# Kernel tuning notes

Hardware: AMD Instinct MI355X
Metric: run time of the kernel (lower is better)

## Reference

```python
import jax, jax.numpy as jnp
import numpy as np

N_EMBD = 512
Q_N_EMBD = 512
N_HEAD = 8
EPS = 1e-5


def _layernorm(x, w, b):
    mu = jnp.mean(x, axis=-1, keepdims=True)
    var = jnp.mean(jnp.square(x - mu), axis=-1, keepdims=True)
    return (x - mu) * jax.lax.rsqrt(var + EPS) * w + b


def setup_inputs() -> dict:
    key = jax.random.key(0)
    ks = jax.random.split(key, 16)
    B, C, H, W = 8, N_EMBD, 32, 32
    s = 1.0 / np.sqrt(N_EMBD)
    inp = {
        "q": jax.random.normal(ks[0], (B, Q_N_EMBD, H, W), jnp.float32),
        "kv": jax.random.normal(ks[1], (B, C, H, W), jnp.float32),
        "ln_kv_w": jnp.ones((N_EMBD,), jnp.float32),
        "ln_kv_b": jnp.zeros((N_EMBD,), jnp.float32),
        "ln_q_w": jnp.ones((Q_N_EMBD,), jnp.float32),
        "ln_q_b": jnp.zeros((Q_N_EMBD,), jnp.float32),
        "Wk": jax.random.normal(ks[2], (N_EMBD, N_EMBD), jnp.float32) * s,
        "bk": jnp.zeros((N_EMBD,), jnp.float32),
        "Wq": jax.random.normal(ks[3], (Q_N_EMBD, N_EMBD), jnp.float32) * s,
        "bq": jnp.zeros((N_EMBD,), jnp.float32),
        "Wv": jax.random.normal(ks[4], (N_EMBD, N_EMBD), jnp.float32) * s,
        "bv": jnp.zeros((N_EMBD,), jnp.float32),
        "Wp": jax.random.normal(ks[5], (N_EMBD, N_EMBD), jnp.float32) * s,
        "bp": jnp.zeros((N_EMBD,), jnp.float32),
    }
    return inp


def reference(q, kv, ln_kv_w, ln_kv_b, ln_q_w, ln_q_b,
              Wk, bk, Wq, bq, Wv, bv, Wp, bp):
    B, C, H, W = kv.shape
    c_q = q.shape[1]
    T = H * W
    hd = C // N_HEAD  # head dim

    # [B, C, H, W] -> [B, T, C] tokens
    kv_t = kv.reshape(B, C, T).transpose(0, 2, 1)
    q_t = q.reshape(B, c_q, T).transpose(0, 2, 1)

    kv_n = _layernorm(kv_t, ln_kv_w, ln_kv_b)
    q_n = _layernorm(q_t, ln_q_w, ln_q_b)

    # projections, split heads: [B, T, C] -> [B, H, T, hd]
    def heads(x):
        return x.reshape(B, T, N_HEAD, hd).transpose(0, 2, 1, 3)

    k = heads(kv_n @ Wk + bk)
    qh = heads(q_n @ Wq + bq)
    v = heads(kv_n @ Wv + bv)

    att = jnp.einsum('bhqd,bhkd->bhqk', qh, k) * (1.0 / np.sqrt(hd))
    att = jax.nn.softmax(att, axis=-1)
    y = jnp.einsum('bhqk,bhkd->bhqd', att, v)
    y = y.transpose(0, 2, 1, 3).reshape(B, T, C)
    y = y @ Wp + bp

    x = kv_t + y  # residual on (pre-LN) kv tokens
    return x.transpose(0, 2, 1).reshape(B, C, H, W)
```

## Files before the change

kernel.cpp:

```cpp
#include <hip/hip_runtime.h>
#include <stdint.h>

#define DI static __device__ __forceinline__

typedef __attribute__((ext_vector_type(8))) short bh8;
typedef __attribute__((ext_vector_type(4))) float f4;

DI short f2bf(float f) {
  unsigned u = __float_as_uint(f);
  u += 0x7fffu + ((u >> 16) & 1u);
  return (short)(u >> 16);
}

DI unsigned pkbf(float a, float b) {
  unsigned ua = __float_as_uint(a) + 0x8000u;
  unsigned ub = __float_as_uint(b) + 0x8000u;
  return __builtin_amdgcn_perm(ub, ua, 0x07060302u);
}

DI unsigned pk4fp8(float a, float b, float c, float d) {
  unsigned w = 0;
  w = __builtin_amdgcn_cvt_pk_fp8_f32(a, b, w, false);
  w = __builtin_amdgcn_cvt_pk_fp8_f32(c, d, w, true);
  return w;
}

DI void gll16(const void* g, void* l) {
  __builtin_amdgcn_global_load_lds(
      (const __attribute__((address_space(1))) unsigned int*)g,
      (__attribute__((address_space(3))) unsigned int*)l, 16, 0, 0);
}

DI f4 mfma16(bh8 a, bh8 b, f4 c) {
  return __builtin_amdgcn_mfma_f32_16x16x32_bf16(a, b, c, 0, 0, 0);
}

DI f4 mfma8(long a, long b, f4 c) {
  return __builtin_amdgcn_mfma_f32_16x16x32_fp8_fp8(a, b, c, 0, 0, 0);
}

DI bh8 ld8(const short* p) { return *(const bh8*)p; }

__global__ __launch_bounds__(256) void prep_k(
    const float* __restrict__ kv, const float* __restrict__ qi,
    const float* __restrict__ kw, const float* __restrict__ kbv,
    const float* __restrict__ qw, const float* __restrict__ qbv,
    const float* __restrict__ Wk, const float* __restrict__ Wq,
    const float* __restrict__ Wv, const float* __restrict__ Wp,
    short* __restrict__ kvn, short* __restrict__ qn,
    short* __restrict__ Wt)
{
  __shared__ char sm[16 * 516 * 4 + 128];
  int role = blockIdx.y;
  int bx = blockIdx.x;
  int tid = threadIdx.x;

  if (role < 4) {
    if (bx >= 256) return;
    float (*ts)[33] = (float(*)[33])sm;
    const float* w = (role == 0) ? Wk : (role == 1) ? Wq : (role == 2) ? Wv : Wp;
    short* o = Wt + ((size_t)role << 18);
    int c0 = (bx & 15) << 5, r0 = (bx >> 4) << 5;
    int tx = tid & 31, ty = tid >> 5;
#pragma unroll
    for (int k = 0; k < 32; k += 8)
      ts[ty + k][tx] = w[((size_t)(r0 + ty + k) << 9) + c0 + tx];
    __syncthreads();
#pragma unroll
    for (int k = 0; k < 32; k += 8)
      o[((size_t)(c0 + ty + k) << 9) + r0 + tx] = f2bf(ts[tx][ty + k]);
    return;
  }

  float (*xs)[516] = (float(*)[516])sm;
  float* smean = (float*)(sm + 16 * 516 * 4);
  float* srstd = smean + 16;
  int which = role - 4;
  const float* x = which ? qi : kv;
  const float* w = which ? qw : kw;
  const float* bb = which ? qbv : kbv;
  short* o = which ? qn : kvn;
  int b = bx >> 6;
  int t0 = (bx & 63) << 4;
  const float* xb = x + ((size_t)b << 19) + (size_t)t0;
#pragma unroll
  for (int k = 0; k < 8; k++) {
    int idx = (k << 8) + tid;
    int c = idx >> 2, tt = (idx & 3) << 2;
    float4 v = *(const float4*)(xb + ((size_t)c << 10) + tt);
    xs[tt + 0][c] = v.x; xs[tt + 1][c] = v.y;
    xs[tt + 2][c] = v.z; xs[tt + 3][c] = v.w;
  }
  __syncthreads();
  {
    int t = tid >> 4, cp = tid & 15;
    float s = 0.f, s2 = 0.f;
#pragma unroll
    for (int k = 0; k < 8; k++) {
      float4 v = *(const float4*)&xs[t][(cp << 2) + (k << 6)];
      s  += v.x + v.y + v.z + v.w;
      s2 += v.x * v.x + v.y * v.y + v.z * v.z + v.w * v.w;
    }
#pragma unroll
    for (int m = 1; m < 16; m <<= 1) {
      s  += __shfl_xor(s,  m);
      s2 += __shfl_xor(s2, m);
    }
    if (cp == 0) {
      float mean = s * (1.f / 512.f);
      float var  = s2 * (1.f / 512.f) - mean * mean;
      smean[t] = mean;
      srstd[t] = rsqrtf(var + 1e-5f);
    }
  }
  __syncthreads();
#pragma unroll
  for (int k = 0; k < 8; k++) {
    int idx = (k << 8) + tid;
    int t = idx >> 7, c = (idx & 127) << 2;
    float4 v = *(const float4*)&xs[t][c];
    float4 wv = *(const float4*)(w + c);
    float4 bv4 = *(const float4*)(bb + c);
    float mu = smean[t], rs = srstd[t];
    float r0 = (v.x - mu) * rs * wv.x + bv4.x;
    float r1 = (v.y - mu) * rs * wv.y + bv4.y;
    float r2 = (v.z - mu) * rs * wv.z + bv4.z;
    float r3 = (v.w - mu) * rs * wv.w + bv4.w;
    uint2 pk; pk.x = pkbf(r0, r1); pk.y = pkbf(r2, r3);
    *(uint2*)(o + (((size_t)(b << 10) + t0 + t) << 9) + c) = pk;
  }
}

__global__ __launch_bounds__(256, 3) void gemm_qkv_k(
    const short* __restrict__ kvn, const short* __restrict__ qn,
    const short* __restrict__ Wt,
    const float* __restrict__ bk, const float* __restrict__ bq,
    const float* __restrict__ bv,
    unsigned char* __restrict__ kb8, unsigned char* __restrict__ qb8,
    unsigned char* __restrict__ vb8)
{
  __shared__ short As[128 * 64];
  __shared__ short Bs[128 * 64];
  int z = blockIdx.z;
  const short* A; const short* Bt; const float* bias;
  int m0, n0;
  if (z == 0)      { A = Wt;             Bt = kvn;            bias = bk; }
  else if (z == 1) { A = Wt + (1 << 18); Bt = qn;             bias = bq; }
  else             { A = kvn;            Bt = Wt + (2 << 18); bias = bv; }
  if (z == 2) { m0 = blockIdx.x << 7; n0 = blockIdx.y << 7; }
  else        { m0 = blockIdx.y << 7; n0 = blockIdx.x << 7; }
  int tid = threadIdx.x;
  int lane = tid & 63, wid = tid >> 6;
  int r = lane & 15, g = lane >> 4;
  int wrow = (wid >> 1) << 6, wcol = (wid & 1) << 6;
  f4 acc[4][4];
#pragma unroll
  for (int i = 0; i < 4; i++)
#pragma unroll
    for (int j = 0; j < 4; j++) {
      acc[i][j][0] = 0.f; acc[i][j][1] = 0.f;
      acc[i][j][2] = 0.f; acc[i][j][3] = 0.f;
    }
  for (int k0 = 0; k0 < 512; k0 += 64) {
    __syncthreads();
#pragma unroll
    for (int it = 0; it < 4; it++) {
      int n = (it << 8) + tid;
      int row = n >> 3;
      int c = (n & 7) ^ (row & 7);
      gll16(A  + ((size_t)(m0 + row) << 9) + k0 + (c << 3), As + (n << 3));
      gll16(Bt + ((size_t)(n0 + row) << 9) + k0 + (c << 3), Bs + (n << 3));
    }
    __syncthreads();
    bh8 a[2][4], b[2][4];
#pragma unroll
    for (int ks = 0; ks < 2; ks++) {
#pragma unroll
      for (int i = 0; i < 4; i++) {
        int R = wrow + (i << 4) + r;
        a[ks][i] = ld8(As + (R << 6) + ((((ks << 2) + g) ^ (R & 7)) << 3));
      }
#pragma unroll
      for (int j = 0; j < 4; j++) {
        int R = wcol + (j << 4) + r;
        b[ks][j] = ld8(Bs + (R << 6) + ((((ks << 2) + g) ^ (R & 7)) << 3));
      }
    }
#pragma unroll
    for (int ks = 0; ks < 2; ks++)
#pragma unroll
      for (int i = 0; i < 4; i++)
#pragma unroll
        for (int j = 0; j < 4; j++)
          acc[i][j] = mfma16(a[ks][i], b[ks][j], acc[i][j]);
  }
#pragma unroll
  for (int i = 0; i < 4; i++) {
#pragma unroll
    for (int j = 0; j < 4; j++) {
      int mm = m0 + wrow + (i << 4) + (g << 2);
      int nn = n0 + wcol + (j << 4) + r;
      if (z == 0) {
        float4 b4 = *(const float4*)(bias + mm);
        int h = mm >> 6, d0 = mm & 63;
        int bb = nn >> 10, tt = nn & 1023;
        int c = tt & 255;
        int p = ((c & 15) << 4) | (c >> 4);
        size_t base = ((size_t)((bb * 8 + h) * 4 + (tt >> 8)) << 14);
        unsigned w = pk4fp8(acc[i][j][0] + b4.x, acc[i][j][1] + b4.y,
                            acc[i][j][2] + b4.z, acc[i][j][3] + b4.w);
        *(unsigned*)(kb8 + base + (p << 6) +
                     (((d0 >> 3) ^ (p & 7)) << 3) + (d0 & 7)) = w;
      } else if (z == 1) {
        float4 b4 = *(const float4*)(bias + mm);
        int h = mm >> 6, d0 = mm & 63;
        int bb = nn >> 10, tt = nn & 1023;
        unsigned w = pk4fp8(acc[i][j][0] + b4.x, acc[i][j][1] + b4.y,
                            acc[i][j][2] + b4.z, acc[i][j][3] + b4.w);
        *(unsigned*)(qb8 + ((((size_t)(bb * 8 + h)) << 10) + tt) * 64 + d0) = w;
      } else {
        float bvv = bias[nn];
        int h = nn >> 6, d = nn & 63;
        int bb = mm >> 10, tt = mm & 1023;
        int t8 = tt & 255;
        int tb = (((t8 >> 4) & 3) << 3) | (((t8 >> 3) & 1) << 2) | (t8 >> 6);
        size_t base = ((size_t)((bb * 8 + h) * 4 + (tt >> 8)) << 14);
        unsigned w = pk4fp8(acc[i][j][0] + bvv, acc[i][j][1] + bvv,
                            acc[i][j][2] + bvv, acc[i][j][3] + bvv);
        *(unsigned*)(vb8 + base + (d << 8) +
                     ((tb ^ (d & 31)) << 3) + (tt & 7)) = w;
      }
    }
  }
}

__global__ __launch_bounds__(256, 3) void gemm_proj_k(
    const short* __restrict__ A, const short* __restrict__ Bt,
    const float* __restrict__ bias, float* __restrict__ outp,
    const float* __restrict__ resid)
{
  __shared__ short As[64 * 64];
  __shared__ short Bs[128 * 64];
  int m0 = blockIdx.y << 6, n0 = blockIdx.x << 7;
  int tid = threadIdx.x;
  int lane = tid & 63, wid = tid >> 6;
  int r = lane & 15, g = lane >> 4;
  int wrow = (wid >> 1) << 5, wcol = (wid & 1) << 6;
  f4 acc[2][4];
#pragma unroll
  for (int i = 0; i < 2; i++)
#pragma unroll
    for (int j = 0; j < 4; j++) {
      acc[i][j][0] = 0.f; acc[i][j][1] = 0.f;
      acc[i][j][2] = 0.f; acc[i][j][3] = 0.f;
    }
  for (int k0 = 0; k0 < 512; k0 += 64) {
    __syncthreads();
#pragma unroll
    for (int it = 0; it < 2; it++) {
      int n = (it << 8) + tid;
      int row = n >> 3;
      int c = (n & 7) ^ (row & 7);
      gll16(A + ((size_t)(m0 + row) << 9) + k0 + (c << 3), As + (n << 3));
    }
#pragma unroll
    for (int it = 0; it < 4; it++) {
      int n = (it << 8) + tid;
      int row = n >> 3;
      int c = (n & 7) ^ (row & 7);
      gll16(Bt + ((size_t)(n0 + row) << 9) + k0 + (c << 3), Bs + (n << 3));
    }
    __syncthreads();
    bh8 a[2][2], b[2][4];
#pragma unroll
    for (int ks = 0; ks < 2; ks++) {
#pragma unroll
      for (int i = 0; i < 2; i++) {
        int R = wrow + (i << 4) + r;
        a[ks][i] = ld8(As + (R << 6) + ((((ks << 2) + g) ^ (R & 7)) << 3));
      }
#pragma unroll
      for (int j = 0; j < 4; j++) {
        int R = wcol + (j << 4) + r;
        b[ks][j] = ld8(Bs + (R << 6) + ((((ks << 2) + g) ^ (R & 7)) << 3));
      }
    }
#pragma unroll
    for (int ks = 0; ks < 2; ks++)
#pragma unroll
      for (int i = 0; i < 2; i++)
#pragma unroll
        for (int j = 0; j < 4; j++)
          acc[i][j] = mfma16(a[ks][i], b[ks][j], acc[i][j]);
  }
#pragma unroll
  for (int i = 0; i < 2; i++) {
#pragma unroll
    for (int j = 0; j < 4; j++) {
      int mm = m0 + wrow + (i << 4) + (g << 2);
      int nn = n0 + wcol + (j << 4) + r;
      int bb = nn >> 10, t = nn & 1023;
#pragma unroll
      for (int q = 0; q < 4; q++) {
        int m = mm + q;
        size_t ad = ((((size_t)bb << 9) + m) << 10) + t;
        outp[ad] = acc[i][j][q] + bias[m] + resid[ad];
      }
    }
  }
}

__global__ __launch_bounds__(256, 4) void attn_k(
    const unsigned char* __restrict__ qb8, const unsigned char* __restrict__ kb8,
    const unsigned char* __restrict__ vb8, short* __restrict__ yo)
{
  __shared__ char Ks[16384];
  __shared__ char Vs[16384];
  int h = blockIdx.x, b = blockIdx.z;
  int qt0 = blockIdx.y << 6;
  int tid = threadIdx.x, lane = tid & 63;
  int r = lane & 15, g = lane >> 4;
  int wbase = (tid >> 6) << 4;
  size_t bh = (size_t)(b * 8 + h);
  const unsigned char* Qg = qb8 + ((bh << 10) + qt0) * 64;
  const unsigned char* Kg = kb8 + (bh << 16);
  const unsigned char* Vg = vb8 + (bh << 16);

  long qf8[2];
#pragma unroll
  for (int ksd = 0; ksd < 2; ksd++)
    qf8[ksd] = *(const long*)(Qg +
        ((size_t)(wbase + r) << 6) + (((ksd << 2) + g) << 3));

  f4 oac[4];
#pragma unroll
  for (int jn = 0; jn < 4; jn++) {
    oac[jn][0] = 0.f; oac[jn][1] = 0.f; oac[jn][2] = 0.f; oac[jn][3] = 0.f;
  }
  float rs = 0.f;

  const float csc = 0.18033688011112042f;

  for (int ck = 0; ck < 4; ck++) {
    __syncthreads();
#pragma unroll
    for (int it = 0; it < 4; it++) {
      int n = ((it << 8) + tid) << 4;
      gll16(Kg + (ck << 14) + n, Ks + n);
      gll16(Vg + (ck << 14) + n, Vs + n);
    }
    __syncthreads();

    unsigned Wq[4][4];
#pragma unroll
    for (int jq = 0; jq < 4; jq++) {
      f4 s[4];
#pragma unroll
      for (int jj = 0; jj < 4; jj++) {
        s[jj][0] = 0.f; s[jj][1] = 0.f; s[jj][2] = 0.f; s[jj][3] = 0.f;
      }
#pragma unroll
      for (int ksd = 0; ksd < 2; ksd++)
#pragma unroll
        for (int jj = 0; jj < 4; jj++) {
          int j = (jq << 2) + jj;
          long kf = *(const long*)(Ks + (((j << 4) + r) << 6) +
                        ((((ksd << 2) + g) ^ (r & 7)) << 3));
          s[jj] = mfma8(kf, qf8[ksd], s[jj]);
        }
#pragma unroll
      for (int qq = 0; qq < 4; qq++) {
        float e0 = __builtin_amdgcn_exp2f(fminf(fmaf(s[0][qq], csc, -3.0f), 8.5f));
        float e1 = __builtin_amdgcn_exp2f(fminf(fmaf(s[1][qq], csc, -3.0f), 8.5f));
        float e2 = __builtin_amdgcn_exp2f(fminf(fmaf(s[2][qq], csc, -3.0f), 8.5f));
        float e3 = __builtin_amdgcn_exp2f(fminf(fmaf(s[3][qq], csc, -3.0f), 8.5f));
        rs += (e0 + e1) + (e2 + e3);
        Wq[qq][jq] = pk4fp8(e0, e1, e2, e3);
      }
    }

#pragma unroll
    for (int ks = 0; ks < 8; ks++) {
      long ap = (long)(unsigned)Wq[ks >> 1][(ks & 1) << 1] |
                ((long)Wq[ks >> 1][((ks & 1) << 1) + 1] << 32);
#pragma unroll
      for (int jn = 0; jn < 4; jn++) {
        int d = (jn << 4) + r;
        long bv8 = *(const long*)(Vs + (d << 8) +
                      ((((ks << 2) + g) ^ (d & 31)) << 3));
        oac[jn] = mfma8(ap, bv8, oac[jn]);
      }
    }
  }

  rs += __shfl_xor(rs, 16);
  rs += __shfl_xor(rs, 32);

#pragma unroll
  for (int qq = 0; qq < 4; qq++) {
    float rsq = __shfl(rs, (g << 2) + qq);
    float inv = 1.f / (rsq + 1e-20f);
    int trow = qt0 + wbase + (g << 2) + qq;
    size_t base = (((size_t)(b << 10) + trow) << 9) + (h << 6);
#pragma unroll
    for (int jn = 0; jn < 4; jn++)
      yo[base + (jn << 4) + r] = f2bf(oac[jn][qq] * inv);
  }
}

extern "C" void kernel_launch(void* const* d_in, const int* in_sizes, int n_in,
                              void* d_out, int out_size, void* d_ws, size_t ws_size,
                              hipStream_t stream)
{
  const float* q    = (const float*)d_in[0];
  const float* kv   = (const float*)d_in[1];
  const float* lnkw = (const float*)d_in[2];
  const float* lnkb = (const float*)d_in[3];
  const float* lnqw = (const float*)d_in[4];
  const float* lnqb = (const float*)d_in[5];
  const float* Wk   = (const float*)d_in[6];
  const float* bk   = (const float*)d_in[7];
  const float* Wq   = (const float*)d_in[8];
  const float* bq   = (const float*)d_in[9];
  const float* Wv   = (const float*)d_in[10];
  const float* bv   = (const float*)d_in[11];
  const float* Wp   = (const float*)d_in[12];
  const float* bp   = (const float*)d_in[13];

  char* ws = (char*)d_ws;
  const size_t SZ = (size_t)8192 * 512 * 2;
  short* buf0 = (short*)(ws);
  short* qn   = (short*)(ws + SZ);
  unsigned char* kb8 = (unsigned char*)(ws + 2 * SZ);
  unsigned char* qb8 = (unsigned char*)(ws + 3 * SZ);
  unsigned char* vb8 = (unsigned char*)(ws + 4 * SZ);
  short* Wt   = (short*)(ws + 5 * SZ);
  if (ws_size < 5 * SZ + 4 * 512 * 512 * 2) return;

  prep_k<<<dim3(512, 6), 256, 0, stream>>>(kv, q, lnkw, lnkb, lnqw, lnqb,
                                           Wk, Wq, Wv, Wp, buf0, qn, Wt);
  gemm_qkv_k<<<dim3(64, 4, 3), 256, 0, stream>>>(buf0, qn, Wt, bk, bq, bv,
                                                 kb8, qb8, vb8);
  attn_k<<<dim3(8, 16, 8), 256, 0, stream>>>(qb8, kb8, vb8, buf0);
  gemm_proj_k<<<dim3(64, 8), 256, 0, stream>>>(Wt + (3 << 18), buf0, bp,
                                               (float*)d_out, kv);
}
```

Measured before the change: 165.5 us.

## Double-buffer LDS tiles in QKV GEMM, projection GEMM and attention kernels

Adds two-stage LDS ping-pong buffering to the QKV GEMM, projection GEMM and attention kernels. The global-to-LDS loads for the next K tile are issued before computing on the current one, and each iteration ends with a single waitcnt plus barrier instead of two syncthreads. This aims to hide global load latency behind MFMA work. In exchange, LDS use doubles and the occupancy hints drop (3 to 2 for QKV, 4 to 2 for attention), which leaves fewer waves per CU to hide latency.

```diff
diff --git a/kernel.cpp b/kernel.cpp
--- a/kernel.cpp
+++ b/kernel.cpp
@@ -29,6 +29,10 @@
   __builtin_amdgcn_global_load_lds(
       (const __attribute__((address_space(1))) unsigned int*)g,
       (__attribute__((address_space(3))) unsigned int*)l, 16, 0, 0);
+}
+
+DI void fence_vm_lgkm() {
+  asm volatile("s_waitcnt vmcnt(0) lgkmcnt(0)" ::: "memory");
 }
 
 DI f4 mfma16(bh8 a, bh8 b, f4 c) {
@@ -131,7 +135,7 @@
   }
 }
 
-__global__ __launch_bounds__(256, 3) void gemm_qkv_k(
+__global__ __launch_bounds__(256, 2) void gemm_qkv_k(
     const short* __restrict__ kvn, const short* __restrict__ qn,
     const short* __restrict__ Wt,
     const float* __restrict__ bk, const float* __restrict__ bq,
@@ -139,8 +143,8 @@
     unsigned char* __restrict__ kb8, unsigned char* __restrict__ qb8,
     unsigned char* __restrict__ vb8)
 {
-  __shared__ short As[128 * 64];
-  __shared__ short Bs[128 * 64];
+  __shared__ short As[2][128 * 64];
+  __shared__ short Bs[2][128 * 64];
   int z = blockIdx.z;
   const short* A; const short* Bt; const float* bias;
   int m0, n0;
@@ -153,37 +157,49 @@
   int lane = tid & 63, wid = tid >> 6;
   int r = lane & 15, g = lane >> 4;
   int wrow = (wid >> 1) << 6, wcol = (wid & 1) << 6;
-  f4 acc[4][4];
-#pragma unroll
-  for (int i = 0; i < 4; i++)
-#pragma unroll
-    for (int j = 0; j < 4; j++) {
-      acc[i][j][0] = 0.f; acc[i][j][1] = 0.f;
-      acc[i][j][2] = 0.f; acc[i][j][3] = 0.f;
-    }
-  for (int k0 = 0; k0 < 512; k0 += 64) {
-    __syncthreads();
+
+  auto STAGE = [&](int k0, int s) {
 #pragma unroll
     for (int it = 0; it < 4; it++) {
       int n = (it << 8) + tid;
       int row = n >> 3;
       int c = (n & 7) ^ (row & 7);
-      gll16(A  + ((size_t)(m0 + row) << 9) + k0 + (c << 3), As + (n << 3));
-      gll16(Bt + ((size_t)(n0 + row) << 9) + k0 + (c << 3), Bs + (n << 3));
-    }
-    __syncthreads();
+      gll16(A  + ((size_t)(m0 + row) << 9) + k0 + (c << 3), &As[s][n << 3]);
+      gll16(Bt + ((size_t)(n0 + row) << 9) + k0 + (c << 3), &Bs[s][n << 3]);
+    }
+  };
+
+  f4 acc[4][4];
+#pragma unroll
+  for (int i = 0; i < 4; i++)
+#pragma unroll
+    for (int j = 0; j < 4; j++) {
+      acc[i][j][0] = 0.f; acc[i][j][1] = 0.f;
+      acc[i][j][2] = 0.f; acc[i][j][3] = 0.f;
+    }
+
+  STAGE(0, 0);
+  fence_vm_lgkm();
+  __builtin_amdgcn_s_barrier();
+  __builtin_amdgcn_sched_barrier(0);
+
+  for (int kt = 0; kt < 8; kt++) {
+    int cur = kt & 1;
+    if (kt < 7) STAGE((kt + 1) << 6, cur ^ 1);
+    const short* Ap = As[cur];
+    const short* Bp = Bs[cur];
     bh8 a[2][4], b[2][4];
 #pragma unroll
     for (int ks = 0; ks < 2; ks++) {
 #pragma unroll
       for (int i = 0; i < 4; i++) {
         int R = wrow + (i << 4) + r;
-        a[ks][i] = ld8(As + (R << 6) + ((((ks << 2) + g) ^ (R & 7)) << 3));
+        a[ks][i] = ld8(Ap + (R << 6) + ((((ks << 2) + g) ^ (R & 7)) << 3));
       }
 #pragma unroll
       for (int j = 0; j < 4; j++) {
         int R = wcol + (j << 4) + r;
-        b[ks][j] = ld8(Bs + (R << 6) + ((((ks << 2) + g) ^ (R & 7)) << 3));
+        b[ks][j] = ld8(Bp + (R << 6) + ((((ks << 2) + g) ^ (R & 7)) << 3));
       }
     }
 #pragma unroll
@@ -193,6 +209,11 @@
 #pragma unroll
         for (int j = 0; j < 4; j++)
           acc[i][j] = mfma16(a[ks][i], b[ks][j], acc[i][j]);
+    if (kt < 7) {
+      fence_vm_lgkm();
+      __builtin_amdgcn_s_barrier();
+      __builtin_amdgcn_sched_barrier(0);
+    }
   }
 #pragma unroll
   for (int i = 0; i < 4; i++) {
@@ -239,50 +260,62 @@
     const float* __restrict__ bias, float* __restrict__ outp,
     const float* __restrict__ resid)
 {
-  __shared__ short As[64 * 64];
-  __shared__ short Bs[128 * 64];
+  __shared__ short As[2][64 * 64];
+  __shared__ short Bs[2][128 * 64];
   int m0 = blockIdx.y << 6, n0 = blockIdx.x << 7;
   int tid = threadIdx.x;
   int lane = tid & 63, wid = tid >> 6;
   int r = lane & 15, g = lane >> 4;
   int wrow = (wid >> 1) << 5, wcol = (wid & 1) << 6;
-  f4 acc[2][4];
-#pragma unroll
-  for (int i = 0; i < 2; i++)
-#pragma unroll
-    for (int j = 0; j < 4; j++) {
-      acc[i][j][0] = 0.f; acc[i][j][1] = 0.f;
-      acc[i][j][2] = 0.f; acc[i][j][3] = 0.f;
-    }
-  for (int k0 = 0; k0 < 512; k0 += 64) {
-    __syncthreads();
+
+  auto STAGE = [&](int k0, int s) {
 #pragma unroll
     for (int it = 0; it < 2; it++) {
       int n = (it << 8) + tid;
       int row = n >> 3;
       int c = (n & 7) ^ (row & 7);
-      gll16(A + ((size_t)(m0 + row) << 9) + k0 + (c << 3), As + (n << 3));
+      gll16(A + ((size_t)(m0 + row) << 9) + k0 + (c << 3), &As[s][n << 3]);
     }
 #pragma unroll
     for (int it = 0; it < 4; it++) {
       int n = (it << 8) + tid;
       int row = n >> 3;
       int c = (n & 7) ^ (row & 7);
-      gll16(Bt + ((size_t)(n0 + row) << 9) + k0 + (c << 3), Bs + (n << 3));
-    }
-    __syncthreads();
+      gll16(Bt + ((size_t)(n0 + row) << 9) + k0 + (c << 3), &Bs[s][n << 3]);
+    }
+  };
+
+  f4 acc[2][4];
+#pragma unroll
+  for (int i = 0; i < 2; i++)
+#pragma unroll
+    for (int j = 0; j < 4; j++) {
+      acc[i][j][0] = 0.f; acc[i][j][1] = 0.f;
+      acc[i][j][2] = 0.f; acc[i][j][3] = 0.f;
+    }
+
+  STAGE(0, 0);
+  fence_vm_lgkm();
+  __builtin_amdgcn_s_barrier();
+  __builtin_amdgcn_sched_barrier(0);
+
+  for (int kt = 0; kt < 8; kt++) {
+    int cur = kt & 1;
+    if (kt < 7) STAGE((kt + 1) << 6, cur ^ 1);
+    const short* Ap = As[cur];
+    const short* Bp = Bs[cur];
     bh8 a[2][2], b[2][4];
 #pragma unroll
     for (int ks = 0; ks < 2; ks++) {
 #pragma unroll
       for (int i = 0; i < 2; i++) {
         int R = wrow + (i << 4) + r;
-        a[ks][i] = ld8(As + (R << 6) + ((((ks << 2) + g) ^ (R & 7)) << 3));
+        a[ks][i] = ld8(Ap + (R << 6) + ((((ks << 2) + g) ^ (R & 7)) << 3));
       }
 #pragma unroll
       for (int j = 0; j < 4; j++) {
         int R = wcol + (j << 4) + r;
-        b[ks][j] = ld8(Bs + (R << 6) + ((((ks << 2) + g) ^ (R & 7)) << 3));
+        b[ks][j] = ld8(Bp + (R << 6) + ((((ks << 2) + g) ^ (R & 7)) << 3));
       }
     }
 #pragma unroll
@@ -292,6 +325,11 @@
 #pragma unroll
         for (int j = 0; j < 4; j++)
           acc[i][j] = mfma16(a[ks][i], b[ks][j], acc[i][j]);
+    if (kt < 7) {
+      fence_vm_lgkm();
+      __builtin_amdgcn_s_barrier();
+      __builtin_amdgcn_sched_barrier(0);
+    }
   }
 #pragma unroll
   for (int i = 0; i < 2; i++) {
@@ -310,12 +348,12 @@
   }
 }
 
-__global__ __launch_bounds__(256, 4) void attn_k(
+__global__ __launch_bounds__(256, 2) void attn_k(
     const unsigned char* __restrict__ qb8, const unsigned char* __restrict__ kb8,
     const unsigned char* __restrict__ vb8, short* __restrict__ yo)
 {
-  __shared__ char Ks[16384];
-  __shared__ char Vs[16384];
+  __shared__ char Ks[2][16384];
+  __shared__ char Vs[2][16384];
   int h = blockIdx.x, b = blockIdx.z;
   int qt0 = blockIdx.y << 6;
   int tid = threadIdx.x, lane = tid & 63;
@@ -326,6 +364,15 @@
   const unsigned char* Kg = kb8 + (bh << 16);
   const unsigned char* Vg = vb8 + (bh << 16);
 
+  auto STAGE = [&](int ck, int s) {
+#pragma unroll
+    for (int it = 0; it < 4; it++) {
+      int n = ((it << 8) + tid) << 4;
+      gll16(Kg + (ck << 14) + n, &Ks[s][n]);
+      gll16(Vg + (ck << 14) + n, &Vs[s][n]);
+    }
+  };
+
   long qf8[2];
 #pragma unroll
   for (int ksd = 0; ksd < 2; ksd++)
@@ -341,15 +388,16 @@
 
   const float csc = 0.18033688011112042f;
 
+  STAGE(0, 0);
+  fence_vm_lgkm();
+  __builtin_amdgcn_s_barrier();
+  __builtin_amdgcn_sched_barrier(0);
+
   for (int ck = 0; ck < 4; ck++) {
-    __syncthreads();
-#pragma unroll
-    for (int it = 0; it < 4; it++) {
-      int n = ((it << 8) + tid) << 4;
-      gll16(Kg + (ck << 14) + n, Ks + n);
-      gll16(Vg + (ck << 14) + n, Vs + n);
-    }
-    __syncthreads();
+    int cur = ck & 1;
+    if (ck < 3) STAGE(ck + 1, cur ^ 1);
+    const char* Kp = Ks[cur];
+    const char* Vp = Vs[cur];
 
     unsigned Wq[4][4];
 #pragma unroll
@@ -364,7 +412,7 @@
 #pragma unroll
         for (int jj = 0; jj < 4; jj++) {
           int j = (jq << 2) + jj;
-          long kf = *(const long*)(Ks + (((j << 4) + r) << 6) +
+          long kf = *(const long*)(Kp + (((j << 4) + r) << 6) +
                         ((((ksd << 2) + g) ^ (r & 7)) << 3));
           s[jj] = mfma8(kf, qf8[ksd], s[jj]);
         }
@@ -386,10 +434,16 @@
 #pragma unroll
       for (int jn = 0; jn < 4; jn++) {
         int d = (jn << 4) + r;
-        long bv8 = *(const long*)(Vs + (d << 8) +
+        long bv8 = *(const long*)(Vp + (d << 8) +
                       ((((ks << 2) + g) ^ (d & 31)) << 3));
         oac[jn] = mfma8(ap, bv8, oac[jn]);
       }
+    }
+
+    if (ck < 3) {
+      fence_vm_lgkm();
+      __builtin_amdgcn_s_barrier();
+      __builtin_amdgcn_sched_barrier(0);
     }
   }
 
```

Measured after the change: 176.2 us. +6.5%, slower.

## Process two query tiles per attention block to reuse staged K/V

Applied to the files above, without the earlier changes.

Each attention block now handles 128 query rows instead of 64, with each wave running two 16-row query sub-tiles against the same K/V fragments loaded from shared memory. This halves the number of blocks and halves the global-to-LDS traffic for K and V per query, and reuses each K and V register fragment for two MFMAs. In exchange register pressure roughly doubles for accumulators (launch bounds lowered to 3 blocks/SM) and the grid shrinks to 512 blocks, which may reduce occupancy and latency hiding.

```diff
diff --git a/kernel.cpp b/kernel.cpp
--- a/kernel.cpp
+++ b/kernel.cpp
@@ -310,14 +310,14 @@
   }
 }
 
-__global__ __launch_bounds__(256, 4) void attn_k(
+__global__ __launch_bounds__(256, 3) void attn_k(
     const unsigned char* __restrict__ qb8, const unsigned char* __restrict__ kb8,
     const unsigned char* __restrict__ vb8, short* __restrict__ yo)
 {
   __shared__ char Ks[16384];
   __shared__ char Vs[16384];
   int h = blockIdx.x, b = blockIdx.z;
-  int qt0 = blockIdx.y << 6;
+  int qt0 = blockIdx.y << 7;
   int tid = threadIdx.x, lane = tid & 63;
   int r = lane & 15, g = lane >> 4;
   int wbase = (tid >> 6) << 4;
@@ -326,18 +326,23 @@
   const unsigned char* Kg = kb8 + (bh << 16);
   const unsigned char* Vg = vb8 + (bh << 16);
 
-  long qf8[2];
-#pragma unroll
-  for (int ksd = 0; ksd < 2; ksd++)
-    qf8[ksd] = *(const long*)(Qg +
-        ((size_t)(wbase + r) << 6) + (((ksd << 2) + g) << 3));
-
-  f4 oac[4];
-#pragma unroll
-  for (int jn = 0; jn < 4; jn++) {
-    oac[jn][0] = 0.f; oac[jn][1] = 0.f; oac[jn][2] = 0.f; oac[jn][3] = 0.f;
-  }
-  float rs = 0.f;
+  long qf8[2][2];
+#pragma unroll
+  for (int u = 0; u < 2; u++)
+#pragma unroll
+    for (int ksd = 0; ksd < 2; ksd++)
+      qf8[u][ksd] = *(const long*)(Qg +
+          ((size_t)((u << 6) + wbase + r) << 6) + (((ksd << 2) + g) << 3));
+
+  f4 oac[2][4];
+#pragma unroll
+  for (int u = 0; u < 2; u++)
+#pragma unroll
+    for (int jn = 0; jn < 4; jn++) {
+      oac[u][jn][0] = 0.f; oac[u][jn][1] = 0.f;
+      oac[u][jn][2] = 0.f; oac[u][jn][3] = 0.f;
+    }
+  float rs[2] = {0.f, 0.f};
 
   const float csc = 0.18033688011112042f;
 
@@ -351,14 +356,17 @@
     }
     __syncthreads();
 
-    unsigned Wq[4][4];
+    unsigned Wq2[2][4][4];
 #pragma unroll
     for (int jq = 0; jq < 4; jq++) {
-      f4 s[4];
-#pragma unroll
-      for (int jj = 0; jj < 4; jj++) {
-        s[jj][0] = 0.f; s[jj][1] = 0.f; s[jj][2] = 0.f; s[jj][3] = 0.f;
-      }
+      f4 s2[2][4];
+#pragma unroll
+      for (int u = 0; u < 2; u++)
+#pragma unroll
+        for (int jj = 0; jj < 4; jj++) {
+          s2[u][jj][0] = 0.f; s2[u][jj][1] = 0.f;
+          s2[u][jj][2] = 0.f; s2[u][jj][3] = 0.f;
+        }
 #pragma unroll
       for (int ksd = 0; ksd < 2; ksd++)
 #pragma unroll
@@ -366,46 +374,57 @@
           int j = (jq << 2) + jj;
           long kf = *(const long*)(Ks + (((j << 4) + r) << 6) +
                         ((((ksd << 2) + g) ^ (r & 7)) << 3));
-          s[jj] = mfma8(kf, qf8[ksd], s[jj]);
+          s2[0][jj] = mfma8(kf, qf8[0][ksd], s2[0][jj]);
+          s2[1][jj] = mfma8(kf, qf8[1][ksd], s2[1][jj]);
         }
 #pragma unroll
-      for (int qq = 0; qq < 4; qq++) {
-        float e0 = __builtin_amdgcn_exp2f(fminf(fmaf(s[0][qq], csc, -3.0f), 8.5f));
-        float e1 = __builtin_amdgcn_exp2f(fminf(fmaf(s[1][qq], csc, -3.0f), 8.5f));
-        float e2 = __builtin_amdgcn_exp2f(fminf(fmaf(s[2][qq], csc, -3.0f), 8.5f));
-        float e3 = __builtin_amdgcn_exp2f(fminf(fmaf(s[3][qq], csc, -3.0f), 8.5f));
-        rs += (e0 + e1) + (e2 + e3);
-        Wq[qq][jq] = pk4fp8(e0, e1, e2, e3);
-      }
+      for (int u = 0; u < 2; u++)
+#pragma unroll
+        for (int qq = 0; qq < 4; qq++) {
+          float e0 = __builtin_amdgcn_exp2f(fminf(fmaf(s2[u][0][qq], csc, -3.0f), 8.5f));
+          float e1 = __builtin_amdgcn_exp2f(fminf(fmaf(s2[u][1][qq], csc, -3.0f), 8.5f));
+          float e2 = __builtin_amdgcn_exp2f(fminf(fmaf(s2[u][2][qq], csc, -3.0f), 8.5f));
+          float e3 = __builtin_amdgcn_exp2f(fminf(fmaf(s2[u][3][qq], csc, -3.0f), 8.5f));
+          rs[u] += (e0 + e1) + (e2 + e3);
+          Wq2[u][qq][jq] = pk4fp8(e0, e1, e2, e3);
+        }
     }
 
 #pragma unroll
     for (int ks = 0; ks < 8; ks++) {
-      long ap = (long)(unsigned)Wq[ks >> 1][(ks & 1) << 1] |
-                ((long)Wq[ks >> 1][((ks & 1) << 1) + 1] << 32);
 #pragma unroll
       for (int jn = 0; jn < 4; jn++) {
         int d = (jn << 4) + r;
         long bv8 = *(const long*)(Vs + (d << 8) +
                       ((((ks << 2) + g) ^ (d & 31)) << 3));
-        oac[jn] = mfma8(ap, bv8, oac[jn]);
-      }
-    }
-  }
-
-  rs += __shfl_xor(rs, 16);
-  rs += __shfl_xor(rs, 32);
-
-#pragma unroll
-  for (int qq = 0; qq < 4; qq++) {
-    float rsq = __shfl(rs, (g << 2) + qq);
-    float inv = 1.f / (rsq + 1e-20f);
-    int trow = qt0 + wbase + (g << 2) + qq;
-    size_t base = (((size_t)(b << 10) + trow) << 9) + (h << 6);
-#pragma unroll
-    for (int jn = 0; jn < 4; jn++)
-      yo[base + (jn << 4) + r] = f2bf(oac[jn][qq] * inv);
-  }
+#pragma unroll
+        for (int u = 0; u < 2; u++) {
+          long ap = (long)(unsigned)Wq2[u][ks >> 1][(ks & 1) << 1] |
+                    ((long)Wq2[u][ks >> 1][((ks & 1) << 1) + 1] << 32);
+          oac[u][jn] = mfma8(ap, bv8, oac[u][jn]);
+        }
+      }
+    }
+  }
+
+#pragma unroll
+  for (int u = 0; u < 2; u++) {
+    rs[u] += __shfl_xor(rs[u], 16);
+    rs[u] += __shfl_xor(rs[u], 32);
+  }
+
+#pragma unroll
+  for (int u = 0; u < 2; u++)
+#pragma unroll
+    for (int qq = 0; qq < 4; qq++) {
+      float rsq = __shfl(rs[u], (g << 2) + qq);
+      float inv = 1.f / (rsq + 1e-20f);
+      int trow = qt0 + (u << 6) + wbase + (g << 2) + qq;
+      size_t base = (((size_t)(b << 10) + trow) << 9) + (h << 6);
+#pragma unroll
+      for (int jn = 0; jn < 4; jn++)
+        yo[base + (jn << 4) + r] = f2bf(oac[u][jn][qq] * inv);
+    }
 }
 
 extern "C" void kernel_launch(void* const* d_in, const int* in_sizes, int n_in,
@@ -441,7 +460,7 @@
                                            Wk, Wq, Wv, Wp, buf0, qn, Wt);
   gemm_qkv_k<<<dim3(64, 4, 3), 256, 0, stream>>>(buf0, qn, Wt, bk, bq, bv,
                                                  kb8, qb8, vb8);
-  attn_k<<<dim3(8, 16, 8), 256, 0, stream>>>(qb8, kb8, vb8, buf0);
+  attn_k<<<dim3(8, 8, 8), 256, 0, stream>>>(qb8, kb8, vb8, buf0);
   gemm_proj_k<<<dim3(64, 8), 256, 0, stream>>>(Wt + (3 << 18), buf0, bp,
                                                (float*)d_out, kv);
 }
```

New measurement: 169.8 us. 1.03x slower.

## Fuse K and V projections into one GEMM block sharing the kv tile

Applied to the files above, without the earlier changes.

The K and V projections, which both read the normalized kv activations, are merged into a single block. It loads the kv tile once and multiplies it against both Wk and Wv tiles, keeping two accumulator sets. This drops a separate V grid slice and halves the kv activation traffic for those projections. In exchange, register pressure rises (launch bounds go from 3 to 2 blocks per CU), shared memory grows, and V is now written as scattered single-byte fp8 stores instead of packed 4-byte stores.

```diff
diff --git a/kernel.cpp b/kernel.cpp
--- a/kernel.cpp
+++ b/kernel.cpp
@@ -23,6 +23,10 @@
   w = __builtin_amdgcn_cvt_pk_fp8_f32(a, b, w, false);
   w = __builtin_amdgcn_cvt_pk_fp8_f32(c, d, w, true);
   return w;
+}
+
+DI unsigned char fp8of(float x) {
+  return (unsigned char)(__builtin_amdgcn_cvt_pk_fp8_f32(x, 0.f, 0, false) & 0xff);
 }
 
 DI void gll16(const void* g, void* l) {
@@ -131,7 +135,7 @@
   }
 }
 
-__global__ __launch_bounds__(256, 3) void gemm_qkv_k(
+__global__ __launch_bounds__(256, 2) void gemm_qkv_k(
     const short* __restrict__ kvn, const short* __restrict__ qn,
     const short* __restrict__ Wt,
     const float* __restrict__ bk, const float* __restrict__ bq,
@@ -140,95 +144,148 @@
     unsigned char* __restrict__ vb8)
 {
   __shared__ short As[128 * 64];
+  __shared__ short Cs[128 * 64];
   __shared__ short Bs[128 * 64];
   int z = blockIdx.z;
-  const short* A; const short* Bt; const float* bias;
-  int m0, n0;
-  if (z == 0)      { A = Wt;             Bt = kvn;            bias = bk; }
-  else if (z == 1) { A = Wt + (1 << 18); Bt = qn;             bias = bq; }
-  else             { A = kvn;            Bt = Wt + (2 << 18); bias = bv; }
-  if (z == 2) { m0 = blockIdx.x << 7; n0 = blockIdx.y << 7; }
-  else        { m0 = blockIdx.y << 7; n0 = blockIdx.x << 7; }
+  int m0 = blockIdx.y << 7, n0 = blockIdx.x << 7;
   int tid = threadIdx.x;
   int lane = tid & 63, wid = tid >> 6;
   int r = lane & 15, g = lane >> 4;
   int wrow = (wid >> 1) << 6, wcol = (wid & 1) << 6;
-  f4 acc[4][4];
-#pragma unroll
-  for (int i = 0; i < 4; i++)
-#pragma unroll
-    for (int j = 0; j < 4; j++) {
-      acc[i][j][0] = 0.f; acc[i][j][1] = 0.f;
-      acc[i][j][2] = 0.f; acc[i][j][3] = 0.f;
-    }
-  for (int k0 = 0; k0 < 512; k0 += 64) {
-    __syncthreads();
-#pragma unroll
-    for (int it = 0; it < 4; it++) {
-      int n = (it << 8) + tid;
-      int row = n >> 3;
-      int c = (n & 7) ^ (row & 7);
-      gll16(A  + ((size_t)(m0 + row) << 9) + k0 + (c << 3), As + (n << 3));
-      gll16(Bt + ((size_t)(n0 + row) << 9) + k0 + (c << 3), Bs + (n << 3));
-    }
-    __syncthreads();
-    bh8 a[2][4], b[2][4];
-#pragma unroll
-    for (int ks = 0; ks < 2; ks++) {
-#pragma unroll
-      for (int i = 0; i < 4; i++) {
-        int R = wrow + (i << 4) + r;
-        a[ks][i] = ld8(As + (R << 6) + ((((ks << 2) + g) ^ (R & 7)) << 3));
-      }
+
+  if (z == 0) {
+    const short* A1 = Wt;
+    const short* A2 = Wt + (2 << 18);
+    f4 acc1[4][4], acc2[4][4];
+#pragma unroll
+    for (int i = 0; i < 4; i++)
 #pragma unroll
       for (int j = 0; j < 4; j++) {
-        int R = wcol + (j << 4) + r;
-        b[ks][j] = ld8(Bs + (R << 6) + ((((ks << 2) + g) ^ (R & 7)) << 3));
-      }
-    }
-#pragma unroll
-    for (int ks = 0; ks < 2; ks++)
-#pragma unroll
-      for (int i = 0; i < 4; i++)
-#pragma unroll
-        for (int j = 0; j < 4; j++)
-          acc[i][j] = mfma16(a[ks][i], b[ks][j], acc[i][j]);
-  }
-#pragma unroll
-  for (int i = 0; i < 4; i++) {
-#pragma unroll
-    for (int j = 0; j < 4; j++) {
-      int mm = m0 + wrow + (i << 4) + (g << 2);
-      int nn = n0 + wcol + (j << 4) + r;
-      if (z == 0) {
-        float4 b4 = *(const float4*)(bias + mm);
+        acc1[i][j][0] = 0.f; acc1[i][j][1] = 0.f;
+        acc1[i][j][2] = 0.f; acc1[i][j][3] = 0.f;
+        acc2[i][j][0] = 0.f; acc2[i][j][1] = 0.f;
+        acc2[i][j][2] = 0.f; acc2[i][j][3] = 0.f;
+      }
+    for (int k0 = 0; k0 < 512; k0 += 64) {
+      __syncthreads();
+#pragma unroll
+      for (int it = 0; it < 4; it++) {
+        int n = (it << 8) + tid;
+        int row = n >> 3;
+        int c = (n & 7) ^ (row & 7);
+        gll16(A1  + ((size_t)(m0 + row) << 9) + k0 + (c << 3), As + (n << 3));
+        gll16(A2  + ((size_t)(m0 + row) << 9) + k0 + (c << 3), Cs + (n << 3));
+        gll16(kvn + ((size_t)(n0 + row) << 9) + k0 + (c << 3), Bs + (n << 3));
+      }
+      __syncthreads();
+#pragma unroll
+      for (int ks = 0; ks < 2; ks++) {
+        bh8 bfr[4], a1[4], a2[4];
+#pragma unroll
+        for (int j = 0; j < 4; j++) {
+          int R = wcol + (j << 4) + r;
+          bfr[j] = ld8(Bs + (R << 6) + ((((ks << 2) + g) ^ (R & 7)) << 3));
+        }
+#pragma unroll
+        for (int i = 0; i < 4; i++) {
+          int R = wrow + (i << 4) + r;
+          a1[i] = ld8(As + (R << 6) + ((((ks << 2) + g) ^ (R & 7)) << 3));
+          a2[i] = ld8(Cs + (R << 6) + ((((ks << 2) + g) ^ (R & 7)) << 3));
+        }
+#pragma unroll
+        for (int i = 0; i < 4; i++)
+#pragma unroll
+          for (int j = 0; j < 4; j++) {
+            acc1[i][j] = mfma16(a1[i], bfr[j], acc1[i][j]);
+            acc2[i][j] = mfma16(a2[i], bfr[j], acc2[i][j]);
+          }
+      }
+    }
+#pragma unroll
+    for (int i = 0; i < 4; i++) {
+#pragma unroll
+      for (int j = 0; j < 4; j++) {
+        int mm = m0 + wrow + (i << 4) + (g << 2);
+        int nn = n0 + wcol + (j << 4) + r;
         int h = mm >> 6, d0 = mm & 63;
         int bb = nn >> 10, tt = nn & 1023;
-        int c = tt & 255;
-        int p = ((c & 15) << 4) | (c >> 4);
         size_t base = ((size_t)((bb * 8 + h) * 4 + (tt >> 8)) << 14);
-        unsigned w = pk4fp8(acc[i][j][0] + b4.x, acc[i][j][1] + b4.y,
-                            acc[i][j][2] + b4.z, acc[i][j][3] + b4.w);
-        *(unsigned*)(kb8 + base + (p << 6) +
-                     (((d0 >> 3) ^ (p & 7)) << 3) + (d0 & 7)) = w;
-      } else if (z == 1) {
-        float4 b4 = *(const float4*)(bias + mm);
+        {
+          float4 b4 = *(const float4*)(bk + mm);
+          int c = tt & 255;
+          int p = ((c & 15) << 4) | (c >> 4);
+          unsigned w = pk4fp8(acc1[i][j][0] + b4.x, acc1[i][j][1] + b4.y,
+                              acc1[i][j][2] + b4.z, acc1[i][j][3] + b4.w);
+          *(unsigned*)(kb8 + base + (p << 6) +
+                       (((d0 >> 3) ^ (p & 7)) << 3) + (d0 & 7)) = w;
+        }
+        {
+          float4 b4 = *(const float4*)(bv + mm);
+          int t8 = tt & 255;
+          int tb = (((t8 >> 4) & 3) << 3) | (((t8 >> 3) & 1) << 2) | (t8 >> 6);
+          const float* bp4 = (const float*)&b4;
+#pragma unroll
+          for (int qv = 0; qv < 4; qv++) {
+            int d = d0 + qv;
+            vb8[base + (d << 8) + ((tb ^ (d & 31)) << 3) + (t8 & 7)] =
+                fp8of(acc2[i][j][qv] + bp4[qv]);
+          }
+        }
+      }
+    }
+  } else {
+    const short* A = Wt + (1 << 18);
+    f4 acc[4][4];
+#pragma unroll
+    for (int i = 0; i < 4; i++)
+#pragma unroll
+      for (int j = 0; j < 4; j++) {
+        acc[i][j][0] = 0.f; acc[i][j][1] = 0.f;
+        acc[i][j][2] = 0.f; acc[i][j][3] = 0.f;
+      }
+    for (int k0 = 0; k0 < 512; k0 += 64) {
+      __syncthreads();
+#pragma unroll
+      for (int it = 0; it < 4; it++) {
+        int n = (it << 8) + tid;
+        int row = n >> 3;
+        int c = (n & 7) ^ (row & 7);
+        gll16(A  + ((size_t)(m0 + row) << 9) + k0 + (c << 3), As + (n << 3));
+        gll16(qn + ((size_t)(n0 + row) << 9) + k0 + (c << 3), Bs + (n << 3));
+      }
+      __syncthreads();
+#pragma unroll
+      for (int ks = 0; ks < 2; ks++) {
+        bh8 bfr[4], a1[4];
+#pragma unroll
+        for (int j = 0; j < 4; j++) {
+          int R = wcol + (j << 4) + r;
+          bfr[j] = ld8(Bs + (R << 6) + ((((ks << 2) + g) ^ (R & 7)) << 3));
+        }
+#pragma unroll
+        for (int i = 0; i < 4; i++) {
+          int R = wrow + (i << 4) + r;
+          a1[i] = ld8(As + (R << 6) + ((((ks << 2) + g) ^ (R & 7)) << 3));
+        }
+#pragma unroll
+        for (int i = 0; i < 4; i++)
+#pragma unroll
+          for (int j = 0; j < 4; j++)
+            acc[i][j] = mfma16(a1[i], bfr[j], acc[i][j]);
+      }
+    }
+#pragma unroll
+    for (int i = 0; i < 4; i++) {
+#pragma unroll
+      for (int j = 0; j < 4; j++) {
+        int mm = m0 + wrow + (i << 4) + (g << 2);
+        int nn = n0 + wcol + (j << 4) + r;
+        float4 b4 = *(const float4*)(bq + mm);
         int h = mm >> 6, d0 = mm & 63;
         int bb = nn >> 10, tt = nn & 1023;
         unsigned w = pk4fp8(acc[i][j][0] + b4.x, acc[i][j][1] + b4.y,
                             acc[i][j][2] + b4.z, acc[i][j][3] + b4.w);
         *(unsigned*)(qb8 + ((((size_t)(bb * 8 + h)) << 10) + tt) * 64 + d0) = w;
-      } else {
-        float bvv = bias[nn];
-        int h = nn >> 6, d = nn & 63;
-        int bb = mm >> 10, tt = mm & 1023;
-        int t8 = tt & 255;
-        int tb = (((t8 >> 4) & 3) << 3) | (((t8 >> 3) & 1) << 2) | (t8 >> 6);
-        size_t base = ((size_t)((bb * 8 + h) * 4 + (tt >> 8)) << 14);
-        unsigned w = pk4fp8(acc[i][j][0] + bvv, acc[i][j][1] + bvv,
-                            acc[i][j][2] + bvv, acc[i][j][3] + bvv);
-        *(unsigned*)(vb8 + base + (d << 8) +
-                     ((tb ^ (d & 31)) << 3) + (tt & 7)) = w;
       }
     }
   }
@@ -439,7 +496,7 @@
 
   prep_k<<<dim3(512, 6), 256, 0, stream>>>(kv, q, lnkw, lnkb, lnqw, lnqb,
                                            Wk, Wq, Wv, Wp, buf0, qn, Wt);
-  gemm_qkv_k<<<dim3(64, 4, 3), 256, 0, stream>>>(buf0, qn, Wt, bk, bq, bv,
+  gemm_qkv_k<<<dim3(64, 4, 2), 256, 0, stream>>>(buf0, qn, Wt, bk, bq, bv,
                                                  kb8, qb8, vb8);
   attn_k<<<dim3(8, 16, 8), 256, 0, stream>>>(qb8, kb8, vb8, buf0);
   gemm_proj_k<<<dim3(64, 8), 256, 0, stream>>>(Wt + (3 << 18), buf0, bp,
```

New measurement: 167.6 us. Within noise of the previous version (+1.3%).
